# Kernel tuning notes

Measured on AMD Instinct MI355X. Metric: run time of the kernel, lower is better.

The kernel has to match this reference:

```python
import jax, jax.numpy as jnp
import numpy as np

N = 50000
E = 800000
D_IN, D_HID, D_OUT = 128, 128, 64


def gcn_layer(x, src, dst, W, b, n_nodes):
    # GCNConv: h = W x; add self-loops; symmetric normalization deg^-1/2;
    # scatter-add messages from src to dst; add bias.
    h = x @ W  # [N, d_out]
    loop = jnp.arange(n_nodes, dtype=src.dtype)
    src_sl = jnp.concatenate([src, loop])  # [E+N]
    dst_sl = jnp.concatenate([dst, loop])
    deg = jax.ops.segment_sum(jnp.ones_like(dst_sl, dtype=h.dtype), dst_sl,
                              num_segments=n_nodes)  # in-degree incl. self-loop
    dis = jnp.where(deg > 0, jax.lax.rsqrt(deg), 0.0)
    norm = dis[src_sl] * dis[dst_sl]  # [E+N]
    msg = h[src_sl] * norm[:, None]  # gather + scale
    out = jax.ops.segment_sum(msg, dst_sl, num_segments=n_nodes)
    return out + b


def setup_inputs() -> dict:
    key = jax.random.key(0)
    ks = jax.random.split(key, 8)
    x = jax.random.normal(ks[0], (N, D_IN), dtype=jnp.float32)
    edge_index = jax.random.randint(ks[1], (2, E), 0, N, dtype=jnp.int32)
    def glorot(k, fan_in, fan_out):
        s = jnp.sqrt(6.0 / (fan_in + fan_out))
        return jax.random.uniform(k, (fan_in, fan_out), jnp.float32, -s, s)
    return {
        "x": x,
        "edge_index": edge_index,
        "W1": glorot(ks[2], D_IN, D_HID),  "b1": jnp.zeros((D_HID,), jnp.float32),
        "W2": glorot(ks[3], D_HID, D_HID), "b2": jnp.zeros((D_HID,), jnp.float32),
        "W3": glorot(ks[4], D_HID, D_OUT), "b3": jnp.zeros((D_OUT,), jnp.float32),
    }


def reference(x, edge_index, W1, b1, W2, b2, W3, b3):
    src, dst = edge_index[0], edge_index[1]
    n = x.shape[0]
    h = jax.nn.relu(gcn_layer(x, src, dst, W1, b1, n))
    h = jax.nn.relu(gcn_layer(h, src, dst, W2, b2, n))
    return gcn_layer(h, src, dst, W3, b3, n)
```

## Files before the change

kernel.cpp:

```cpp
#include <hip/hip_runtime.h>
#include <hip/hip_fp16.h>
#include <math.h>


__global__ void count_kernel(const int* __restrict__ dst, int* __restrict__ counts,
                             int* __restrict__ rank, int E) {
    int i = blockIdx.x * blockDim.x + threadIdx.x;
    int st = gridDim.x * blockDim.x;
    for (; i < E; i += st) rank[i] = atomicAdd(&counts[dst[i]], 1);
}

__global__ __launch_bounds__(256) void block_sum_kernel(const int* __restrict__ counts,
                                                        int* __restrict__ bsum, int n) {
    const int b = blockIdx.x;
    const int t = threadIdx.x;
    const int idx = b * 256 + t;
    int v = (idx < n) ? counts[idx] : 0;
#pragma unroll
    for (int o = 32; o > 0; o >>= 1) v += __shfl_down(v, o, 64);
    __shared__ int ws[4];
    if ((t & 63) == 0) ws[t >> 6] = v;
    __syncthreads();
    if (t == 0) bsum[b] = ws[0] + ws[1] + ws[2] + ws[3];
}

__global__ __launch_bounds__(256) void small_scan_kernel(int* __restrict__ bsum, int nb) {
    __shared__ int sm[256];
    const int t = threadIdx.x;
    int v = (t < nb) ? bsum[t] : 0;
    sm[t] = v;
    __syncthreads();
    for (int o = 1; o < 256; o <<= 1) {
        int x = (t >= o) ? sm[t - o] : 0;
        __syncthreads();
        sm[t] += x;
        __syncthreads();
    }
    if (t < nb) bsum[t] = sm[t] - v;
}

__global__ __launch_bounds__(256) void scan_block_kernel(const int* __restrict__ counts,
                                                         const int* __restrict__ bsum,
                                                         int* __restrict__ offs,
                                                         float* __restrict__ dis,
                                                         int n, int E) {
    const int b = blockIdx.x;
    const int t = threadIdx.x;
    const int idx = b * 256 + t;
    int v = (idx < n) ? counts[idx] : 0;
    if (idx < n) dis[idx] = rsqrtf((float)(v + 1));
    __shared__ int sm[256];
    sm[t] = v;
    __syncthreads();
    for (int o = 1; o < 256; o <<= 1) {
        int x = (t >= o) ? sm[t - o] : 0;
        __syncthreads();
        sm[t] += x;
        __syncthreads();
    }
    if (idx < n) offs[idx] = bsum[b] + sm[t] - v;
    if (idx == n) offs[n] = E;
}

__global__ void fill_kernel(const int* __restrict__ src, const int* __restrict__ dst,
                            const int* __restrict__ offs, const int* __restrict__ rank,
                            int* __restrict__ csr_s, int E) {
    int i = blockIdx.x * blockDim.x + threadIdx.x;
    int st = gridDim.x * blockDim.x;
    for (; i < E; i += st) {
        int p = offs[dst[i]] + rank[i];
        csr_s[p] = src[i];
    }
}

template <int NOUT>
__global__ __launch_bounds__(256) void gemm_kernel(const float* __restrict__ X,
                                                   const float* __restrict__ W,
                                                   const float* __restrict__ dis,
                                                   __half* __restrict__ Y, int nrows) {
    __shared__ float Ws[128 * NOUT];
    __shared__ float Xs[32 * 128];
    const int t = threadIdx.x;

    {
        const float4* W4 = (const float4*)W;
        float4* Ws4 = (float4*)Ws;
        constexpr int WV = 128 * NOUT / 4;
        for (int i = t; i < WV; i += 256) Ws4[i] = W4[i];
    }
    const int row0 = blockIdx.x * 32;
    {
        float4* Xs4 = (float4*)Xs;
        const float4* X4 = (const float4*)X;
        for (int i = t; i < 32 * 128 / 4; i += 256) {
            int r = i >> 5;
            int rr = row0 + r;
            float4 v = make_float4(0.f, 0.f, 0.f, 0.f);
            if (rr < nrows) v = X4[(size_t)rr * 32 + (i & 31)];
            Xs4[i] = v;
        }
    }
    __syncthreads();

    constexpr int CPT = NOUT / 32;
    const int tr = t >> 5;
    const int tcv = t & 31;

    float acc[4][CPT];
#pragma unroll
    for (int i = 0; i < 4; ++i)
#pragma unroll
        for (int j = 0; j < CPT; ++j) acc[i][j] = 0.f;

    const float4* Xs4 = (const float4*)Xs;

    for (int k = 0; k < 128; k += 4) {
        float4 a[4];
#pragma unroll
        for (int i = 0; i < 4; ++i) a[i] = Xs4[(size_t)(tr * 4 + i) * 32 + (k >> 2)];
#pragma unroll
        for (int kk = 0; kk < 4; ++kk) {
            if constexpr (CPT == 4) {
                float4 b = ((const float4*)Ws)[(size_t)(k + kk) * 32 + tcv];
#pragma unroll
                for (int i = 0; i < 4; ++i) {
                    float av = reinterpret_cast<const float*>(&a[i])[kk];
                    acc[i][0] = fmaf(av, b.x, acc[i][0]);
                    acc[i][1] = fmaf(av, b.y, acc[i][1]);
                    acc[i][2] = fmaf(av, b.z, acc[i][2]);
                    acc[i][3] = fmaf(av, b.w, acc[i][3]);
                }
            } else {
                float2 b = ((const float2*)Ws)[(size_t)(k + kk) * 32 + tcv];
#pragma unroll
                for (int i = 0; i < 4; ++i) {
                    float av = reinterpret_cast<const float*>(&a[i])[kk];
                    acc[i][0] = fmaf(av, b.x, acc[i][0]);
                    acc[i][1] = fmaf(av, b.y, acc[i][1]);
                }
            }
        }
    }

#pragma unroll
    for (int i = 0; i < 4; ++i) {
        int row = row0 + tr * 4 + i;
        if (row < nrows) {
            float dd = dis[row];
            if constexpr (CPT == 4) {
                __half2 p0 = __floats2half2_rn(dd * acc[i][0], dd * acc[i][1]);
                __half2 p1 = __floats2half2_rn(dd * acc[i][2], dd * acc[i][3]);
                uint2 u;
                u.x = *reinterpret_cast<unsigned*>(&p0);
                u.y = *reinterpret_cast<unsigned*>(&p1);
                ((uint2*)Y)[(size_t)row * 32 + tcv] = u;
            } else {
                __half2 p0 = __floats2half2_rn(dd * acc[i][0], dd * acc[i][1]);
                ((unsigned*)Y)[(size_t)row * 32 + tcv] =
                    *reinterpret_cast<unsigned*>(&p0);
            }
        }
    }
}

template <int F, bool RELU>
__global__ __launch_bounds__(256) void agg_kernel(const __half* __restrict__ h,
                                                  const float* __restrict__ dis,
                                                  const int* __restrict__ offs,
                                                  const int* __restrict__ csr_s,
                                                  const float* __restrict__ bias,
                                                  float* __restrict__ out, int n) {
    const int d = blockIdx.x * 4 + (threadIdx.x >> 6);
    if (d >= n) return;
    const int lane = threadIdx.x & 63;
    const int beg = offs[d];
    const int end = offs[d + 1];

    float sx = 0.f, sy = 0.f;
    int i = beg;
    if constexpr (F == 128) {
        const unsigned* h32 = (const unsigned*)h;
        for (; i + 8 <= end; i += 8) {
            int s[8];
#pragma unroll
            for (int j = 0; j < 8; ++j) s[j] = csr_s[i + j];
            unsigned v[8];
#pragma unroll
            for (int j = 0; j < 8; ++j) v[j] = h32[(size_t)s[j] * 64 + lane];
#pragma unroll
            for (int j = 0; j < 8; ++j) {
                float2 vf = __half22float2(*reinterpret_cast<__half2*>(&v[j]));
                sx += vf.x;
                sy += vf.y;
            }
        }
        if (i + 4 <= end) {
            int s[4];
#pragma unroll
            for (int j = 0; j < 4; ++j) s[j] = csr_s[i + j];
            unsigned v[4];
#pragma unroll
            for (int j = 0; j < 4; ++j) v[j] = h32[(size_t)s[j] * 64 + lane];
#pragma unroll
            for (int j = 0; j < 4; ++j) {
                float2 vf = __half22float2(*reinterpret_cast<__half2*>(&v[j]));
                sx += vf.x;
                sy += vf.y;
            }
            i += 4;
        }
        for (; i < end; ++i) {
            unsigned v = h32[(size_t)csr_s[i] * 64 + lane];
            float2 vf = __half22float2(*reinterpret_cast<__half2*>(&v));
            sx += vf.x;
            sy += vf.y;
        }
        {
            unsigned v = h32[(size_t)d * 64 + lane];
            float2 vf = __half22float2(*reinterpret_cast<__half2*>(&v));
            sx += vf.x;
            sy += vf.y;
        }
        float dd = dis[d];
        float2 b2 = ((const float2*)bias)[lane];
        float rx = fmaf(dd, sx, b2.x);
        float ry = fmaf(dd, sy, b2.y);
        if (RELU) {
            rx = fmaxf(rx, 0.f);
            ry = fmaxf(ry, 0.f);
        }
        ((float2*)(out + (size_t)d * F))[lane] = make_float2(rx, ry);
    } else {
        const unsigned short* h16 = (const unsigned short*)h;
        for (; i + 8 <= end; i += 8) {
            int s[8];
#pragma unroll
            for (int j = 0; j < 8; ++j) s[j] = csr_s[i + j];
            unsigned short v[8];
#pragma unroll
            for (int j = 0; j < 8; ++j) v[j] = h16[(size_t)s[j] * 64 + lane];
#pragma unroll
            for (int j = 0; j < 8; ++j)
                sx += __half2float(*reinterpret_cast<__half*>(&v[j]));
        }
        if (i + 4 <= end) {
            int s[4];
#pragma unroll
            for (int j = 0; j < 4; ++j) s[j] = csr_s[i + j];
            unsigned short v[4];
#pragma unroll
            for (int j = 0; j < 4; ++j) v[j] = h16[(size_t)s[j] * 64 + lane];
#pragma unroll
            for (int j = 0; j < 4; ++j)
                sx += __half2float(*reinterpret_cast<__half*>(&v[j]));
            i += 4;
        }
        for (; i < end; ++i) {
            unsigned short v = h16[(size_t)csr_s[i] * 64 + lane];
            sx += __half2float(*reinterpret_cast<__half*>(&v));
        }
        {
            unsigned short v = h16[(size_t)d * 64 + lane];
            sx += __half2float(*reinterpret_cast<__half*>(&v));
        }
        float dd = dis[d];
        float r = fmaf(dd, sx, bias[lane]);
        if (RELU) r = fmaxf(r, 0.f);
        out[(size_t)d * F + lane] = r;
    }
}


extern "C" void kernel_launch(void* const* d_in, const int* in_sizes, int n_in,
                              void* d_out, int out_size, void* d_ws, size_t ws_size,
                              hipStream_t stream) {
    const float* x  = (const float*)d_in[0];
    const int*   ei = (const int*)d_in[1];
    const float* W1 = (const float*)d_in[2];
    const float* b1 = (const float*)d_in[3];
    const float* W2 = (const float*)d_in[4];
    const float* b2 = (const float*)d_in[5];
    const float* W3 = (const float*)d_in[6];
    const float* b3 = (const float*)d_in[7];

    const int N = in_sizes[0] / 128;
    const int E = in_sizes[1] / 2;
    const int* src = ei;
    const int* dst = ei + E;
    float* out = (float*)d_out;

    char* w = (char*)d_ws;
    auto take = [&](size_t bytes) -> void* {
        void* p = (void*)w;
        w += (bytes + 255) & ~(size_t)255;
        return p;
    };
    int*    counts = (int*)take((size_t)N * 4);
    int*    offs   = (int*)take((size_t)(N + 1) * 4);
    float*  dis    = (float*)take((size_t)N * 4);
    int*    bsum   = (int*)take((size_t)1024 * 4);
    int*    csr_s  = (int*)take((size_t)E * 4);
    __half* G16    = (__half*)take((size_t)N * 128 * 2);
    float*  H      = (float*)take((size_t)N * 128 * 4);
    int*    rank   = (int*)G16;

    const int NBLK = (N + 256) / 256;

    hipMemsetAsync(counts, 0, (size_t)N * 4, stream);
    count_kernel<<<2048, 256, 0, stream>>>(dst, counts, rank, E);
    block_sum_kernel<<<NBLK, 256, 0, stream>>>(counts, bsum, N);
    small_scan_kernel<<<1, 256, 0, stream>>>(bsum, NBLK);
    scan_block_kernel<<<NBLK, 256, 0, stream>>>(counts, bsum, offs, dis, N, E);
    fill_kernel<<<2048, 256, 0, stream>>>(src, dst, offs, rank, csr_s, E);

    const int gblocks = (N + 31) / 32;
    const int ablocks = (N + 3) / 4;

    gemm_kernel<128><<<gblocks, 256, 0, stream>>>(x, W1, dis, G16, N);
    agg_kernel<128, true><<<ablocks, 256, 0, stream>>>(G16, dis, offs, csr_s, b1, H, N);
    gemm_kernel<128><<<gblocks, 256, 0, stream>>>(H, W2, dis, G16, N);
    agg_kernel<128, true><<<ablocks, 256, 0, stream>>>(G16, dis, offs, csr_s, b2, H, N);
    gemm_kernel<64><<<gblocks, 256, 0, stream>>>(H, W3, dis, G16, N);
    agg_kernel<64, false><<<ablocks, 256, 0, stream>>>(G16, dis, offs, csr_s, b3, out, N);
}
```

Before: 258.7 us.

## Replace FP32 SIMT GEMM with split-FP16 MFMA GEMM and split-precision activations

Replaces the shared-memory FP32 FMA GEMM with an MFMA 16x16x32 f16 kernel. It emulates near-FP32 accuracy by splitting inputs and weights into hi/lo half pairs and summing three products. The aggregation kernels now write activations directly as hi/lo halves, and new prepass kernels split x and the transposed weights. This targets the GEMM compute cost, at the price of extra split passes, two extra N x 128 half buffers, and scalar fp16 output stores.

```diff
diff --git a/kernel.cpp b/kernel.cpp
--- a/kernel.cpp
+++ b/kernel.cpp
@@ -2,6 +2,9 @@
 #include <hip/hip_fp16.h>
 #include <math.h>
 
+
+typedef _Float16 half8 __attribute__((ext_vector_type(8)));
+typedef float f32x4 __attribute__((ext_vector_type(4)));
 
 __global__ void count_kernel(const int* __restrict__ dst, int* __restrict__ counts,
                              int* __restrict__ rank, int E) {
@@ -73,103 +76,131 @@
     }
 }
 
+__global__ void xsplit_kernel(const float* __restrict__ in, _Float16* __restrict__ hi,
+                              _Float16* __restrict__ lo, int n8) {
+    int i = blockIdx.x * blockDim.x + threadIdx.x;
+    int st = gridDim.x * blockDim.x;
+    const float4* in4 = (const float4*)in;
+    for (; i < n8; i += st) {
+        float4 v0 = in4[(size_t)i * 2];
+        float4 v1 = in4[(size_t)i * 2 + 1];
+        float v[8] = {v0.x, v0.y, v0.z, v0.w, v1.x, v1.y, v1.z, v1.w};
+        half8 h, l;
+#pragma unroll
+        for (int j = 0; j < 8; ++j) {
+            _Float16 hh = (_Float16)v[j];
+            h[j] = hh;
+            l[j] = (_Float16)(v[j] - (float)hh);
+        }
+        ((half8*)hi)[i] = h;
+        ((half8*)lo)[i] = l;
+    }
+}
+
+__global__ __launch_bounds__(256) void wsplit_kernel(const float* __restrict__ W1,
+                                                     const float* __restrict__ W2,
+                                                     const float* __restrict__ W3,
+                                                     _Float16* __restrict__ hi,
+                                                     _Float16* __restrict__ lo) {
+    int idx = blockIdx.x * 256 + threadIdx.x;
+    if (idx >= 40960) return;
+    float v;
+    if (idx < 16384) {
+        int c = idx >> 7, k = idx & 127;
+        v = W1[k * 128 + c];
+    } else if (idx < 32768) {
+        int j = idx - 16384;
+        int c = j >> 7, k = j & 127;
+        v = W2[k * 128 + c];
+    } else {
+        int j = idx - 32768;
+        int c = j >> 7, k = j & 127;
+        v = W3[k * 64 + c];
+    }
+    _Float16 h = (_Float16)v;
+    hi[idx] = h;
+    lo[idx] = (_Float16)(v - (float)h);
+}
+
 template <int NOUT>
-__global__ __launch_bounds__(256) void gemm_kernel(const float* __restrict__ X,
-                                                   const float* __restrict__ W,
-                                                   const float* __restrict__ dis,
-                                                   __half* __restrict__ Y, int nrows) {
-    __shared__ float Ws[128 * NOUT];
-    __shared__ float Xs[32 * 128];
-    const int t = threadIdx.x;
-
-    {
-        const float4* W4 = (const float4*)W;
-        float4* Ws4 = (float4*)Ws;
-        constexpr int WV = 128 * NOUT / 4;
-        for (int i = t; i < WV; i += 256) Ws4[i] = W4[i];
-    }
-    const int row0 = blockIdx.x * 32;
-    {
-        float4* Xs4 = (float4*)Xs;
-        const float4* X4 = (const float4*)X;
-        for (int i = t; i < 32 * 128 / 4; i += 256) {
-            int r = i >> 5;
-            int rr = row0 + r;
-            float4 v = make_float4(0.f, 0.f, 0.f, 0.f);
-            if (rr < nrows) v = X4[(size_t)rr * 32 + (i & 31)];
-            Xs4[i] = v;
-        }
-    }
-    __syncthreads();
-
-    constexpr int CPT = NOUT / 32;
-    const int tr = t >> 5;
-    const int tcv = t & 31;
-
-    float acc[4][CPT];
-#pragma unroll
-    for (int i = 0; i < 4; ++i)
-#pragma unroll
-        for (int j = 0; j < CPT; ++j) acc[i][j] = 0.f;
-
-    const float4* Xs4 = (const float4*)Xs;
-
-    for (int k = 0; k < 128; k += 4) {
-        float4 a[4];
-#pragma unroll
-        for (int i = 0; i < 4; ++i) a[i] = Xs4[(size_t)(tr * 4 + i) * 32 + (k >> 2)];
-#pragma unroll
-        for (int kk = 0; kk < 4; ++kk) {
-            if constexpr (CPT == 4) {
-                float4 b = ((const float4*)Ws)[(size_t)(k + kk) * 32 + tcv];
-#pragma unroll
-                for (int i = 0; i < 4; ++i) {
-                    float av = reinterpret_cast<const float*>(&a[i])[kk];
-                    acc[i][0] = fmaf(av, b.x, acc[i][0]);
-                    acc[i][1] = fmaf(av, b.y, acc[i][1]);
-                    acc[i][2] = fmaf(av, b.z, acc[i][2]);
-                    acc[i][3] = fmaf(av, b.w, acc[i][3]);
-                }
-            } else {
-                float2 b = ((const float2*)Ws)[(size_t)(k + kk) * 32 + tcv];
-#pragma unroll
-                for (int i = 0; i < 4; ++i) {
-                    float av = reinterpret_cast<const float*>(&a[i])[kk];
-                    acc[i][0] = fmaf(av, b.x, acc[i][0]);
-                    acc[i][1] = fmaf(av, b.y, acc[i][1]);
+__global__ __launch_bounds__(256) void gemm_mfma(const _Float16* __restrict__ Xhi,
+                                                 const _Float16* __restrict__ Xlo,
+                                                 const _Float16* __restrict__ WThi,
+                                                 const _Float16* __restrict__ WTlo,
+                                                 const float* __restrict__ dis,
+                                                 _Float16* __restrict__ Y, int nrows) {
+    constexpr int CT = NOUT / 16;
+    const int wave = threadIdx.x >> 6;
+    const int lane = threadIdx.x & 63;
+    const int lrow = lane & 15;
+    const int lk = lane >> 4;
+    const int r0 = (blockIdx.x * 4 + wave) * 32;
+
+    const f32x4 Z = {0.f, 0.f, 0.f, 0.f};
+    f32x4 acc[2][CT];
+#pragma unroll
+    for (int a = 0; a < 2; ++a)
+#pragma unroll
+        for (int b = 0; b < CT; ++b) acc[a][b] = Z;
+
+    const half8* XhiV = (const half8*)Xhi;
+    const half8* XloV = (const half8*)Xlo;
+    const half8* WhiV = (const half8*)WThi;
+    const half8* WloV = (const half8*)WTlo;
+
+    int ar0 = r0 + lrow;
+    int ar1 = r0 + 16 + lrow;
+    if (ar0 > nrows - 1) ar0 = nrows - 1;
+    if (ar1 > nrows - 1) ar1 = nrows - 1;
+
+#pragma unroll
+    for (int ks = 0; ks < 4; ++ks) {
+        const int kidx = ks * 4 + lk;
+        half8 a0h = XhiV[(size_t)ar0 * 16 + kidx];
+        half8 a0l = XloV[(size_t)ar0 * 16 + kidx];
+        half8 a1h = XhiV[(size_t)ar1 * 16 + kidx];
+        half8 a1l = XloV[(size_t)ar1 * 16 + kidx];
+#pragma unroll
+        for (int ct = 0; ct < CT; ++ct) {
+            const size_t bidx = (size_t)(ct * 16 + lrow) * 16 + kidx;
+            half8 bh = WhiV[bidx];
+            half8 bl = WloV[bidx];
+            acc[0][ct] = __builtin_amdgcn_mfma_f32_16x16x32_f16(a0l, bh, acc[0][ct], 0, 0, 0);
+            acc[0][ct] = __builtin_amdgcn_mfma_f32_16x16x32_f16(a0h, bl, acc[0][ct], 0, 0, 0);
+            acc[0][ct] = __builtin_amdgcn_mfma_f32_16x16x32_f16(a0h, bh, acc[0][ct], 0, 0, 0);
+            acc[1][ct] = __builtin_amdgcn_mfma_f32_16x16x32_f16(a1l, bh, acc[1][ct], 0, 0, 0);
+            acc[1][ct] = __builtin_amdgcn_mfma_f32_16x16x32_f16(a1h, bl, acc[1][ct], 0, 0, 0);
+            acc[1][ct] = __builtin_amdgcn_mfma_f32_16x16x32_f16(a1h, bh, acc[1][ct], 0, 0, 0);
+        }
+    }
+
+    const int orow = r0 + lk * 4;
+#pragma unroll
+    for (int rt = 0; rt < 2; ++rt) {
+#pragma unroll
+        for (int r = 0; r < 4; ++r) {
+            int row = orow + rt * 16 + r;
+            if (row < nrows) {
+                float dd = dis[row];
+#pragma unroll
+                for (int ct = 0; ct < CT; ++ct) {
+                    Y[(size_t)row * NOUT + ct * 16 + lrow] =
+                        (_Float16)(dd * acc[rt][ct][r]);
                 }
             }
         }
     }
-
-#pragma unroll
-    for (int i = 0; i < 4; ++i) {
-        int row = row0 + tr * 4 + i;
-        if (row < nrows) {
-            float dd = dis[row];
-            if constexpr (CPT == 4) {
-                __half2 p0 = __floats2half2_rn(dd * acc[i][0], dd * acc[i][1]);
-                __half2 p1 = __floats2half2_rn(dd * acc[i][2], dd * acc[i][3]);
-                uint2 u;
-                u.x = *reinterpret_cast<unsigned*>(&p0);
-                u.y = *reinterpret_cast<unsigned*>(&p1);
-                ((uint2*)Y)[(size_t)row * 32 + tcv] = u;
-            } else {
-                __half2 p0 = __floats2half2_rn(dd * acc[i][0], dd * acc[i][1]);
-                ((unsigned*)Y)[(size_t)row * 32 + tcv] =
-                    *reinterpret_cast<unsigned*>(&p0);
-            }
-        }
-    }
-}
-
-template <int F, bool RELU>
+}
+
+template <int F, bool RELU, bool SPLIT>
 __global__ __launch_bounds__(256) void agg_kernel(const __half* __restrict__ h,
                                                   const float* __restrict__ dis,
                                                   const int* __restrict__ offs,
                                                   const int* __restrict__ csr_s,
                                                   const float* __restrict__ bias,
-                                                  float* __restrict__ out, int n) {
+                                                  float* __restrict__ outf,
+                                                  __half* __restrict__ ohi,
+                                                  __half* __restrict__ olo, int n) {
     const int d = blockIdx.x * 4 + (threadIdx.x >> 6);
     if (d >= n) return;
     const int lane = threadIdx.x & 63;
@@ -229,7 +260,15 @@
             rx = fmaxf(rx, 0.f);
             ry = fmaxf(ry, 0.f);
         }
-        ((float2*)(out + (size_t)d * F))[lane] = make_float2(rx, ry);
+        if constexpr (SPLIT) {
+            __half hx = __float2half(rx), hy = __float2half(ry);
+            __half lx = __float2half(rx - __half2float(hx));
+            __half ly = __float2half(ry - __half2float(hy));
+            ((__half2*)(ohi + (size_t)d * F))[lane] = __halves2half2(hx, hy);
+            ((__half2*)(olo + (size_t)d * F))[lane] = __halves2half2(lx, ly);
+        } else {
+            ((float2*)(outf + (size_t)d * F))[lane] = make_float2(rx, ry);
+        }
     } else {
         const unsigned short* h16 = (const unsigned short*)h;
         for (; i + 8 <= end; i += 8) {
@@ -266,7 +305,14 @@
         float dd = dis[d];
         float r = fmaf(dd, sx, bias[lane]);
         if (RELU) r = fmaxf(r, 0.f);
-        out[(size_t)d * F + lane] = r;
+        out_store:
+        if constexpr (SPLIT) {
+            __half hx = __float2half(r);
+            ohi[(size_t)d * F + lane] = hx;
+            olo[(size_t)d * F + lane] = __float2half(r - __half2float(hx));
+        } else {
+            outf[(size_t)d * F + lane] = r;
+        }
     }
 }
 
@@ -295,14 +341,17 @@
         w += (bytes + 255) & ~(size_t)255;
         return p;
     };
-    int*    counts = (int*)take((size_t)N * 4);
-    int*    offs   = (int*)take((size_t)(N + 1) * 4);
-    float*  dis    = (float*)take((size_t)N * 4);
-    int*    bsum   = (int*)take((size_t)1024 * 4);
-    int*    csr_s  = (int*)take((size_t)E * 4);
-    __half* G16    = (__half*)take((size_t)N * 128 * 2);
-    float*  H      = (float*)take((size_t)N * 128 * 4);
-    int*    rank   = (int*)G16;
+    int*      counts = (int*)take((size_t)N * 4);
+    int*      offs   = (int*)take((size_t)(N + 1) * 4);
+    float*    dis    = (float*)take((size_t)N * 4);
+    int*      bsum   = (int*)take((size_t)1024 * 4);
+    int*      csr_s  = (int*)take((size_t)E * 4);
+    _Float16* G16    = (_Float16*)take((size_t)N * 128 * 2);
+    _Float16* Xhi    = (_Float16*)take((size_t)N * 128 * 2);
+    _Float16* Xlo    = (_Float16*)take((size_t)N * 128 * 2);
+    _Float16* Whi    = (_Float16*)take((size_t)40960 * 2);
+    _Float16* Wlo    = (_Float16*)take((size_t)40960 * 2);
+    int*      rank   = (int*)G16;
 
     const int NBLK = (N + 256) / 256;
 
@@ -313,13 +362,21 @@
     scan_block_kernel<<<NBLK, 256, 0, stream>>>(counts, bsum, offs, dis, N, E);
     fill_kernel<<<2048, 256, 0, stream>>>(src, dst, offs, rank, csr_s, E);
 
-    const int gblocks = (N + 31) / 32;
+    wsplit_kernel<<<160, 256, 0, stream>>>(W1, W2, W3, Whi, Wlo);
+    xsplit_kernel<<<2048, 256, 0, stream>>>(x, Xhi, Xlo, N * 16);
+
+    const int gblocks = (N + 127) / 128;
     const int ablocks = (N + 3) / 4;
 
-    gemm_kernel<128><<<gblocks, 256, 0, stream>>>(x, W1, dis, G16, N);
-    agg_kernel<128, true><<<ablocks, 256, 0, stream>>>(G16, dis, offs, csr_s, b1, H, N);
-    gemm_kernel<128><<<gblocks, 256, 0, stream>>>(H, W2, dis, G16, N);
-    agg_kernel<128, true><<<ablocks, 256, 0, stream>>>(G16, dis, offs, csr_s, b2, H, N);
-    gemm_kernel<64><<<gblocks, 256, 0, stream>>>(H, W3, dis, G16, N);
-    agg_kernel<64, false><<<ablocks, 256, 0, stream>>>(G16, dis, offs, csr_s, b3, out, N);
-}
+    gemm_mfma<128><<<gblocks, 256, 0, stream>>>(Xhi, Xlo, Whi, Wlo, dis, G16, N);
+    agg_kernel<128, true, true><<<ablocks, 256, 0, stream>>>(
+        (const __half*)G16, dis, offs, csr_s, b1, nullptr, (__half*)Xhi, (__half*)Xlo, N);
+    gemm_mfma<128><<<gblocks, 256, 0, stream>>>(Xhi, Xlo, Whi + 16384, Wlo + 16384,
+                                                dis, G16, N);
+    agg_kernel<128, true, true><<<ablocks, 256, 0, stream>>>(
+        (const __half*)G16, dis, offs, csr_s, b2, nullptr, (__half*)Xhi, (__half*)Xlo, N);
+    gemm_mfma<64><<<gblocks, 256, 0, stream>>>(Xhi, Xlo, Whi + 32768, Wlo + 32768,
+                                               dis, G16, N);
+    agg_kernel<64, false, false><<<ablocks, 256, 0, stream>>>(
+        (const __half*)G16, dis, offs, csr_s, b3, out, nullptr, nullptr, N);
+}
```

Result: faster. 235.5 us (-9.0%).
